# Kernel optimization log

Hardware: AMD Instinct MI355X
Metric: run time of the kernel (lower is better)

## Reference

```python
import jax, jax.numpy as jnp
import numpy as np

EMBED_DIM = 1024
HEAD_DIM = 128

def setup_inputs() -> dict:
    key = jax.random.key(0)
    ks = jax.random.split(key, 7)
    B, S = 4, 2048
    x = jax.random.normal(ks[0], (B, S, EMBED_DIM), dtype=jnp.float32)
    # Linear params: weight [embed_dim, head_dim] (applied as x @ W + b), scaled init
    scale = 1.0 / np.sqrt(EMBED_DIM)
    Wq = jax.random.normal(ks[1], (EMBED_DIM, HEAD_DIM), dtype=jnp.float32) * scale
    Wk = jax.random.normal(ks[2], (EMBED_DIM, HEAD_DIM), dtype=jnp.float32) * scale
    Wv = jax.random.normal(ks[3], (EMBED_DIM, HEAD_DIM), dtype=jnp.float32) * scale
    bq = jax.random.normal(ks[4], (HEAD_DIM,), dtype=jnp.float32) * 0.01
    bk = jax.random.normal(ks[5], (HEAD_DIM,), dtype=jnp.float32) * 0.01
    bv = jax.random.normal(ks[6], (HEAD_DIM,), dtype=jnp.float32) * 0.01
    return {"x": x, "Wq": Wq, "bq": bq, "Wk": Wk, "bk": bk, "Wv": Wv, "bv": bv}

def reference(x, Wq, bq, Wk, bk, Wv, bv):
    # x: [B, S, E]
    S = x.shape[1]
    norm = jnp.asarray(HEAD_DIM ** 0.5, x.dtype)
    q = x @ Wq + bq  # [B, S, D]
    k = x @ Wk + bk
    v = x @ Wv + bv
    scores = jnp.einsum('bsd,btd->bst', q, k) / norm  # [B, S, S]
    causal = jnp.tril(jnp.ones((S, S), dtype=bool))
    scores = jnp.where(causal, scores, -jnp.inf)
    att = jax.nn.softmax(scores, axis=-1)
    return jnp.einsum('bst,btd->bsd', att, v)  # [B, S, D]
```

## Files before the change

### kernel.cpp

```cpp
#include <hip/hip_runtime.h>
#include <hip/hip_bf16.h>

typedef __attribute__((ext_vector_type(8))) short short8;
typedef __attribute__((ext_vector_type(4))) float f32x4;

static __device__ __forceinline__ unsigned short f2bf(float f){
  union { float f; unsigned int u; } v; v.f = f;
  unsigned int r = v.u + 0x7fffu + ((v.u >> 16) & 1u);
  return (unsigned short)(r >> 16);
}

static __device__ __forceinline__ void load_lds16(const unsigned short* g, unsigned short* l){
  __builtin_amdgcn_global_load_lds(
      (const __attribute__((address_space(1))) unsigned int*)(g),
      (__attribute__((address_space(3))) unsigned int*)(l), 16, 0, 0);
}

__global__ void k_prep(const float* __restrict__ x, unsigned short* __restrict__ xb,
                       const float* __restrict__ Wq, const float* __restrict__ Wk,
                       const float* __restrict__ Wv,
                       const float* __restrict__ bq, const float* __restrict__ bk,
                       const float* __restrict__ bv,
                       unsigned short* __restrict__ Wt, float* __restrict__ bias){
  int bx = blockIdx.x;
  int tid = threadIdx.x;
  if (bx < 4096){
    int i = (bx * 256 + tid) * 8;
    float4 a = *(const float4*)(x + i);
    float4 b = *(const float4*)(x + i + 4);
    unsigned short h[8];
    h[0]=f2bf(a.x); h[1]=f2bf(a.y); h[2]=f2bf(a.z); h[3]=f2bf(a.w);
    h[4]=f2bf(b.x); h[5]=f2bf(b.y); h[6]=f2bf(b.z); h[7]=f2bf(b.w);
    *(uint4*)(xb + i) = *(uint4*)h;
  } else {
    int gid = (bx - 4096) * 256 + tid;
    int p = gid >> 17;
    int rem = gid & 131071;
    int d = rem >> 10, e = rem & 1023;
    const float* W = (p==0) ? Wq : ((p==1) ? Wk : Wv);
    Wt[gid] = f2bf(W[e*128 + d]);
    if (gid < 384){
      int pp = gid >> 7, dd = gid & 127;
      bias[gid] = (pp==0) ? bq[dd] : ((pp==1) ? bk[dd] : bv[dd]);
    }
  }
}

__global__ __launch_bounds__(256) void k_gemm_qkv(
    const unsigned short* __restrict__ Xb, const unsigned short* __restrict__ Wt,
    const float* __restrict__ bias,
    unsigned short* __restrict__ Qsw, unsigned short* __restrict__ Ksw,
    unsigned short* __restrict__ Vsw){
  __shared__ __align__(16) char smem[49152];
  float* Lf = (float*)smem;
  int tid = threadIdx.x;
  int mt = blockIdx.x;
  int p  = blockIdx.y;
  int m0 = mt * 64;
  int w = tid >> 6, lane = tid & 63, quad = lane >> 4, l16 = lane & 15;
  int wm = (w >> 1) * 32, wn = (w & 1) * 64;
  f32x4 acc[2][4];
  #pragma unroll
  for (int i=0;i<2;i++)
    #pragma unroll
    for (int j=0;j<4;j++) acc[i][j] = (f32x4){0.f,0.f,0.f,0.f};

  const unsigned short* Wp = Wt + p * (128*1024);
  const unsigned short* Ag = Xb + (m0 + w*16 + (lane>>3))*1024 + (lane&7)*8;
  const unsigned short* Bg = Wp + (w*32 + (lane>>3))*1024 + (lane&7)*8;
  int aoff = (w*16)*64;
  int boff = (w*32)*64;

  auto stage = [&](int sel, int k0){
    unsigned short* Al = (unsigned short*)(smem + sel*24576) + aoff;
    unsigned short* Bl = (unsigned short*)(smem + sel*24576 + 8192) + boff;
    load_lds16(Ag + k0, Al);
    load_lds16(Ag + k0 + 8192, Al + 512);
    #pragma unroll
    for (int s8=0; s8<4; s8++) load_lds16(Bg + k0 + s8*8192, Bl + s8*512);
  };

  stage(0, 0);
  __syncthreads();
  int cur = 0;
  for (int t=0; t<16; t++){
    if (t < 15) stage(cur^1, (t+1)*64);
    const unsigned short* Ac = (const unsigned short*)(smem + cur*24576);
    const unsigned short* Bc = Ac + 4096;
    #pragma unroll
    for (int kk=0; kk<64; kk+=32){
      short8 af[2], bf[4];
      #pragma unroll
      for (int i=0;i<2;i++) af[i] = *(const short8*)(Ac + (wm + i*16 + l16)*64 + kk + quad*8);
      #pragma unroll
      for (int j=0;j<4;j++) bf[j] = *(const short8*)(Bc + (wn + j*16 + l16)*64 + kk + quad*8);
      #pragma unroll
      for (int i=0;i<2;i++)
        #pragma unroll
        for (int j=0;j<4;j++)
          acc[i][j] = __builtin_amdgcn_mfma_f32_16x16x32_bf16(af[i], bf[j], acc[i][j], 0,0,0);
    }
    __syncthreads();
    cur ^= 1;
  }

  const float qscale = 0.08838834764831845f;
  if (p == 2){
    #pragma unroll
    for (int i=0;i<2;i++)
      #pragma unroll
      for (int j=0;j<4;j++){
        int grow0 = m0 + wm + i*16 + quad*4;
        int col = wn + j*16 + l16;
        unsigned short pk[4];
        float bv_ = bias[256 + col];
        #pragma unroll
        for (int r=0;r<4;r++) pk[r] = f2bf(acc[i][j][r] + bv_);
        int bb2 = grow0 >> 11, s = grow0 & 2047;
        int t64 = s >> 6, srem = s & 63;
        int kc2 = srem >> 5, q2 = (srem >> 3) & 3, jj = srem & 7;
        int nt = col >> 4, l2 = col & 15;
        *(uint2*)(Vsw + (bb2*32+t64)*8192 + nt*1024 + kc2*512 + q2*128 + l2*8 + jj) = *(uint2*)pk;
      }
  } else {
    #pragma unroll
    for (int i=0;i<2;i++)
      #pragma unroll
      for (int j=0;j<4;j++)
        #pragma unroll
        for (int r=0;r<4;r++)
          Lf[(wm + i*16 + quad*4 + r)*128 + wn + j*16 + l16] = acc[i][j][r];
    __syncthreads();
    unsigned short* dst = (p==0)? Qsw : Ksw;
    float scale = (p==0)? qscale : 1.0f;
    #pragma unroll
    for (int it=0; it<8; it++){
      int g = it*256 + tid;
      int row = g >> 5, cs = (g & 31)*4;
      f32x4 a = *(const f32x4*)(Lf + row*128 + cs);
      int grow = m0 + row;
      int rt = grow >> 4, m = grow & 15;
      int kc = cs >> 5, q2 = (cs >> 3) & 3, jj = cs & 7;
      unsigned short pk[4];
      #pragma unroll
      for (int k=0;k<4;k++) pk[k] = f2bf((a[k] + bias[p*128+cs+k])*scale);
      *(uint2*)(dst + rt*2048 + kc*512 + q2*128 + m*8 + jj) = *(uint2*)pk;
    }
  }
}

__global__ __launch_bounds__(64) void k_attn(
    const unsigned short* __restrict__ Qsw, const unsigned short* __restrict__ Ksw,
    const unsigned short* __restrict__ Vsw, float* __restrict__ Apart){
  __shared__ __align__(16) unsigned short Pw[16*80];
  int x = blockIdx.x;
  int b = x & 3;
  int t = x >> 2;
  int c = t & 15;
  int qb = 127 - (t >> 4);
  int T64 = (qb >> 2) + 1;
  int nch = (T64 + 1) >> 1;
  if (c >= nch) return;
  int lane = threadIdx.x;
  int quad = lane >> 4, l16 = lane & 15;
  int qs = qb * 16;

  short8 aq[4];
  #pragma unroll
  for (int kc=0;kc<4;kc++)
    aq[kc] = *(const short8*)(Qsw + (b*128 + qb)*2048 + kc*512 + lane*8);

  f32x4 o[8];
  #pragma unroll
  for (int i=0;i<8;i++) o[i] = (f32x4){0.f,0.f,0.f,0.f};
  float mcol = -1e30f;
  float lcol = 0.f;
  short8 ap[2];

  const unsigned short* Kb = Ksw + b*128*2048;
  const unsigned short* Vb = Vsw + b*32*8192;

  int tEnd = (T64 < c*2+2) ? T64 : (c*2+2);
  for (int tt = c*2; tt < tEnd; tt++){
    int t0 = tt * 64;
    f32x4 sc[4];
    #pragma unroll
    for (int nt=0;nt<4;nt++) sc[nt] = (f32x4){0.f,0.f,0.f,0.f};
    __builtin_amdgcn_s_setprio(1);
    #pragma unroll
    for (int nt=0;nt<4;nt++){
      const unsigned short* Kt = Kb + ((t0>>4)+nt)*2048 + lane*8;
      #pragma unroll
      for (int kc=0;kc<4;kc++){
        short8 kf = *(const short8*)(Kt + kc*512);
        sc[nt] = __builtin_amdgcn_mfma_f32_16x16x32_bf16(kf, aq[kc], sc[nt], 0,0,0);
      }
    }
    __builtin_amdgcn_s_setprio(0);
    if (t0 + 63 > qs){
      #pragma unroll
      for (int nt=0;nt<4;nt++){
        int kb_ = t0 + nt*16 + quad*4;
        #pragma unroll
        for (int r=0;r<4;r++)
          if (kb_ + r > qs + l16) sc[nt][r] = -1e30f;
      }
    }
    float mt_ = -1e30f;
    #pragma unroll
    for (int nt=0;nt<4;nt++)
      #pragma unroll
      for (int r=0;r<4;r++) mt_ = fmaxf(mt_, sc[nt][r]);
    mt_ = fmaxf(mt_, __shfl_xor(mt_, 16));
    mt_ = fmaxf(mt_, __shfl_xor(mt_, 32));
    float mn = fmaxf(mcol, mt_);
    float al = __expf(mcol - mn);
    mcol = mn;
    float ls = 0.f;
    #pragma unroll
    for (int nt=0;nt<4;nt++)
      #pragma unroll
      for (int r=0;r<4;r++){
        float pv = __expf(sc[nt][r] - mn);
        sc[nt][r] = pv;
        ls += pv;
      }
    ls += __shfl_xor(ls, 16);
    ls += __shfl_xor(ls, 32);
    lcol = lcol*al + ls;
    #pragma unroll
    for (int r=0;r<4;r++){
      float ar = __shfl(al, quad*4 + r);
      #pragma unroll
      for (int nt=0;nt<8;nt++) o[nt][r] *= ar;
    }
    #pragma unroll
    for (int nt=0;nt<4;nt++){
      unsigned short pk[4];
      #pragma unroll
      for (int r=0;r<4;r++) pk[r] = f2bf(sc[nt][r]);
      *(uint2*)(Pw + l16*80 + nt*16 + quad*4) = *(uint2*)pk;
    }
    ap[0] = *(const short8*)(Pw + l16*80 + quad*8);
    ap[1] = *(const short8*)(Pw + l16*80 + 32 + quad*8);
    const unsigned short* Vt0 = Vb + (t0>>6)*8192 + lane*8;
    __builtin_amdgcn_s_setprio(1);
    #pragma unroll
    for (int nt=0; nt<8; nt++)
      #pragma unroll
      for (int kc2=0;kc2<2;kc2++){
        short8 vf = *(const short8*)(Vt0 + nt*1024 + kc2*512);
        o[nt] = __builtin_amdgcn_mfma_f32_16x16x32_bf16(ap[kc2], vf, o[nt], 0,0,0);
      }
    __builtin_amdgcn_s_setprio(0);
  }

  float* slot = Apart + (size_t)((b*128 + qb)*16 + c) * 2080;
  #pragma unroll
  for (int nt=0;nt<8;nt++)
    #pragma unroll
    for (int r=0;r<4;r++)
      slot[(quad*4 + r)*128 + nt*16 + l16] = o[nt][r];
  if (quad == 0){
    slot[2048 + l16] = mcol;
    slot[2064 + l16] = lcol;
  }
}

__global__ __launch_bounds__(256) void k_acomb(const float* __restrict__ Apart,
                                               float* __restrict__ out){
  int b = blockIdx.x & 3, qb = blockIdx.x >> 2;
  int T64 = (qb >> 2) + 1;
  int nch = (T64 + 1) >> 1;
  const float* base = Apart + (size_t)((b*128 + qb)*16) * 2080;
  int tid = threadIdx.x;
  int row = tid >> 4;
  int c0 = (tid & 15) * 8;
  float m = -1e30f;
  for (int c=0;c<nch;c++) m = fmaxf(m, base[c*2080 + 2048 + row]);
  f32x4 acc[2];
  #pragma unroll
  for (int g=0;g<2;g++) acc[g] = (f32x4){0.f,0.f,0.f,0.f};
  float lsum = 0.f;
  for (int c=0;c<nch;c++){
    float e = __expf(base[c*2080 + 2048 + row] - m);
    lsum += base[c*2080 + 2064 + row] * e;
    #pragma unroll
    for (int g=0;g<2;g++){
      f32x4 v = *(const f32x4*)(base + c*2080 + row*128 + c0 + g*4);
      acc[g] += v * e;
    }
  }
  float inv = 1.0f / lsum;
  float* op = out + (size_t)(b*2048 + qb*16 + row)*128 + c0;
  #pragma unroll
  for (int g=0;g<2;g++){
    f32x4 r = acc[g] * inv;
    *(f32x4*)(op + g*4) = r;
  }
}

extern "C" void kernel_launch(void* const* d_in, const int* in_sizes, int n_in,
                              void* d_out, int out_size, void* d_ws, size_t ws_size,
                              hipStream_t stream) {
  const float* x  = (const float*)d_in[0];
  const float* Wq = (const float*)d_in[1];
  const float* bq = (const float*)d_in[2];
  const float* Wk = (const float*)d_in[3];
  const float* bk = (const float*)d_in[4];
  const float* Wv = (const float*)d_in[5];
  const float* bv = (const float*)d_in[6];
  char* ws = (char*)d_ws;
  unsigned short* Xb   = (unsigned short*)(ws);
  unsigned short* Wt   = (unsigned short*)(ws + 16777216);
  float*          bias = (float*)(ws + 17563648);
  unsigned short* Qsw  = (unsigned short*)(ws + 17565184);
  unsigned short* Ksw  = (unsigned short*)(ws + 19662336);
  unsigned short* Vsw  = (unsigned short*)(ws + 21759488);
  float*          Apart= (float*)(ws + 23856640);
  float* out = (float*)d_out;

  hipLaunchKernelGGL(k_prep,    dim3(5632),    dim3(256), 0, stream,
                     x, Xb, Wq, Wk, Wv, bq, bk, bv, Wt, bias);
  hipLaunchKernelGGL(k_gemm_qkv,dim3(128,3),   dim3(256), 0, stream,
                     Xb, Wt, bias, Qsw, Ksw, Vsw);
  hipLaunchKernelGGL(k_attn,    dim3(8192),    dim3(64),  0, stream, Qsw, Ksw, Vsw, Apart);
  hipLaunchKernelGGL(k_acomb,   dim3(512),     dim3(256), 0, stream, Apart, out);
}
```

Before: 136.8 us.

## Fuse split-K combine into attention kernel via atomic last-block reduction

Removes the separate combine kernel launch. Each attention block publishes its partial result, then increments a per-query-block atomic counter. The last block to finish merges the partials and writes the output. Query blocks with only one chunk skip the scratch buffer and write normalized output directly. This saves a launch and some global traffic, but the final combine now runs on a single 64-thread wave per query block, which adds tail work to the attention kernel.

```diff
diff --git a/kernel.cpp b/kernel.cpp
--- a/kernel.cpp
+++ b/kernel.cpp
@@ -21,7 +21,8 @@
                        const float* __restrict__ Wv,
                        const float* __restrict__ bq, const float* __restrict__ bk,
                        const float* __restrict__ bv,
-                       unsigned short* __restrict__ Wt, float* __restrict__ bias){
+                       unsigned short* __restrict__ Wt, float* __restrict__ bias,
+                       int* __restrict__ cnt){
   int bx = blockIdx.x;
   int tid = threadIdx.x;
   if (bx < 4096){
@@ -43,6 +44,7 @@
       int pp = gid >> 7, dd = gid & 127;
       bias[gid] = (pp==0) ? bq[dd] : ((pp==1) ? bk[dd] : bv[dd]);
     }
+    if (gid < 512) cnt[gid] = 0;
   }
 }
 
@@ -151,7 +153,8 @@
 
 __global__ __launch_bounds__(64) void k_attn(
     const unsigned short* __restrict__ Qsw, const unsigned short* __restrict__ Ksw,
-    const unsigned short* __restrict__ Vsw, float* __restrict__ Apart){
+    const unsigned short* __restrict__ Vsw, float* __restrict__ Apart,
+    int* __restrict__ cnt, float* __restrict__ out){
   __shared__ __align__(16) unsigned short Pw[16*80];
   int x = blockIdx.x;
   int b = x & 3;
@@ -255,7 +258,21 @@
     __builtin_amdgcn_s_setprio(0);
   }
 
-  float* slot = Apart + (size_t)((b*128 + qb)*16 + c) * 2080;
+  int gidx = b*128 + qb;
+
+  if (nch == 1){
+    float linv[4];
+    #pragma unroll
+    for (int r=0;r<4;r++) linv[r] = 1.0f / __shfl(lcol, quad*4 + r);
+    #pragma unroll
+    for (int nt=0;nt<8;nt++)
+      #pragma unroll
+      for (int r=0;r<4;r++)
+        out[(size_t)(b*2048 + qs + quad*4 + r)*128 + nt*16 + l16] = o[nt][r]*linv[r];
+    return;
+  }
+
+  float* slot = Apart + (size_t)(gidx*16 + c) * 2080;
   #pragma unroll
   for (int nt=0;nt<8;nt++)
     #pragma unroll
@@ -265,38 +282,37 @@
     slot[2048 + l16] = mcol;
     slot[2064 + l16] = lcol;
   }
-}
-
-__global__ __launch_bounds__(256) void k_acomb(const float* __restrict__ Apart,
-                                               float* __restrict__ out){
-  int b = blockIdx.x & 3, qb = blockIdx.x >> 2;
-  int T64 = (qb >> 2) + 1;
-  int nch = (T64 + 1) >> 1;
-  const float* base = Apart + (size_t)((b*128 + qb)*16) * 2080;
-  int tid = threadIdx.x;
-  int row = tid >> 4;
-  int c0 = (tid & 15) * 8;
+
+  __threadfence();
+  int old = 0;
+  if (lane == 0) old = atomicAdd(cnt + gidx, 1);
+  old = __shfl(old, 0);
+  if (old != nch - 1) return;
+  __threadfence();
+  const float* base = Apart + (size_t)(gidx*16) * 2080;
+  int row = lane >> 2;
+  int c0 = (lane & 3) * 32;
   float m = -1e30f;
-  for (int c=0;c<nch;c++) m = fmaxf(m, base[c*2080 + 2048 + row]);
-  f32x4 acc[2];
-  #pragma unroll
-  for (int g=0;g<2;g++) acc[g] = (f32x4){0.f,0.f,0.f,0.f};
+  for (int cc=0; cc<nch; cc++) m = fmaxf(m, base[cc*2080 + 2048 + row]);
+  f32x4 acc2[8];
+  #pragma unroll
+  for (int g=0;g<8;g++) acc2[g] = (f32x4){0.f,0.f,0.f,0.f};
   float lsum = 0.f;
-  for (int c=0;c<nch;c++){
-    float e = __expf(base[c*2080 + 2048 + row] - m);
-    lsum += base[c*2080 + 2064 + row] * e;
-    #pragma unroll
-    for (int g=0;g<2;g++){
-      f32x4 v = *(const f32x4*)(base + c*2080 + row*128 + c0 + g*4);
-      acc[g] += v * e;
+  for (int cc=0; cc<nch; cc++){
+    float e = __expf(base[cc*2080 + 2048 + row] - m);
+    lsum += base[cc*2080 + 2064 + row] * e;
+    #pragma unroll
+    for (int g=0;g<8;g++){
+      f32x4 v = *(const f32x4*)(base + cc*2080 + row*128 + c0 + g*4);
+      acc2[g] += v * e;
     }
   }
   float inv = 1.0f / lsum;
   float* op = out + (size_t)(b*2048 + qb*16 + row)*128 + c0;
   #pragma unroll
-  for (int g=0;g<2;g++){
-    f32x4 r = acc[g] * inv;
-    *(f32x4*)(op + g*4) = r;
+  for (int g=0;g<8;g++){
+    f32x4 rr = acc2[g] * inv;
+    *(f32x4*)(op + g*4) = rr;
   }
 }
 
@@ -318,12 +334,13 @@
   unsigned short* Ksw  = (unsigned short*)(ws + 19662336);
   unsigned short* Vsw  = (unsigned short*)(ws + 21759488);
   float*          Apart= (float*)(ws + 23856640);
+  int*            cnt  = (int*)(ws + 92014080);
   float* out = (float*)d_out;
 
   hipLaunchKernelGGL(k_prep,    dim3(5632),    dim3(256), 0, stream,
-                     x, Xb, Wq, Wk, Wv, bq, bk, bv, Wt, bias);
+                     x, Xb, Wq, Wk, Wv, bq, bk, bv, Wt, bias, cnt);
   hipLaunchKernelGGL(k_gemm_qkv,dim3(128,3),   dim3(256), 0, stream,
                      Xb, Wt, bias, Qsw, Ksw, Vsw);
-  hipLaunchKernelGGL(k_attn,    dim3(8192),    dim3(64),  0, stream, Qsw, Ksw, Vsw, Apart);
-  hipLaunchKernelGGL(k_acomb,   dim3(512),     dim3(256), 0, stream, Apart, out);
-}
+  hipLaunchKernelGGL(k_attn,    dim3(8192),    dim3(64),  0, stream,
+                     Qsw, Ksw, Vsw, Apart, cnt, out);
+}
```

New measurement: 319.3 us. 133% more time.

## Drop split-KV attention and combine kernel, one workgroup per query block

Applied to the files above, without the earlier changes.

Removes the split-KV partitioning of the attention kernel, where up to 16 chunks per query block wrote partial outputs that a separate combine kernel merged. Each 64-thread workgroup now walks the full causal key range for its 16-row query block and writes normalized output directly. This drops the partial-buffer traffic and one kernel launch. In exchange it launches only 512 single-wave workgroups with very unequal loop lengths, so parallelism and load balance fall sharply.

```diff
diff --git a/kernel.cpp b/kernel.cpp
--- a/kernel.cpp
+++ b/kernel.cpp
@@ -151,16 +151,12 @@
 
 __global__ __launch_bounds__(64) void k_attn(
     const unsigned short* __restrict__ Qsw, const unsigned short* __restrict__ Ksw,
-    const unsigned short* __restrict__ Vsw, float* __restrict__ Apart){
+    const unsigned short* __restrict__ Vsw, float* __restrict__ out){
   __shared__ __align__(16) unsigned short Pw[16*80];
   int x = blockIdx.x;
   int b = x & 3;
-  int t = x >> 2;
-  int c = t & 15;
-  int qb = 127 - (t >> 4);
+  int qb = x >> 2;
   int T64 = (qb >> 2) + 1;
-  int nch = (T64 + 1) >> 1;
-  if (c >= nch) return;
   int lane = threadIdx.x;
   int quad = lane >> 4, l16 = lane & 15;
   int qs = qb * 16;
@@ -180,8 +176,7 @@
   const unsigned short* Kb = Ksw + b*128*2048;
   const unsigned short* Vb = Vsw + b*32*8192;
 
-  int tEnd = (T64 < c*2+2) ? T64 : (c*2+2);
-  for (int tt = c*2; tt < tEnd; tt++){
+  for (int tt = 0; tt < T64; tt++){
     int t0 = tt * 64;
     f32x4 sc[4];
     #pragma unroll
@@ -255,49 +250,14 @@
     __builtin_amdgcn_s_setprio(0);
   }
 
-  float* slot = Apart + (size_t)((b*128 + qb)*16 + c) * 2080;
+  float linv[4];
+  #pragma unroll
+  for (int r=0;r<4;r++) linv[r] = 1.0f / __shfl(lcol, quad*4 + r);
   #pragma unroll
   for (int nt=0;nt<8;nt++)
     #pragma unroll
     for (int r=0;r<4;r++)
-      slot[(quad*4 + r)*128 + nt*16 + l16] = o[nt][r];
-  if (quad == 0){
-    slot[2048 + l16] = mcol;
-    slot[2064 + l16] = lcol;
-  }
-}
-
-__global__ __launch_bounds__(256) void k_acomb(const float* __restrict__ Apart,
-                                               float* __restrict__ out){
-  int b = blockIdx.x & 3, qb = blockIdx.x >> 2;
-  int T64 = (qb >> 2) + 1;
-  int nch = (T64 + 1) >> 1;
-  const float* base = Apart + (size_t)((b*128 + qb)*16) * 2080;
-  int tid = threadIdx.x;
-  int row = tid >> 4;
-  int c0 = (tid & 15) * 8;
-  float m = -1e30f;
-  for (int c=0;c<nch;c++) m = fmaxf(m, base[c*2080 + 2048 + row]);
-  f32x4 acc[2];
-  #pragma unroll
-  for (int g=0;g<2;g++) acc[g] = (f32x4){0.f,0.f,0.f,0.f};
-  float lsum = 0.f;
-  for (int c=0;c<nch;c++){
-    float e = __expf(base[c*2080 + 2048 + row] - m);
-    lsum += base[c*2080 + 2064 + row] * e;
-    #pragma unroll
-    for (int g=0;g<2;g++){
-      f32x4 v = *(const f32x4*)(base + c*2080 + row*128 + c0 + g*4);
-      acc[g] += v * e;
-    }
-  }
-  float inv = 1.0f / lsum;
-  float* op = out + (size_t)(b*2048 + qb*16 + row)*128 + c0;
-  #pragma unroll
-  for (int g=0;g<2;g++){
-    f32x4 r = acc[g] * inv;
-    *(f32x4*)(op + g*4) = r;
-  }
+      out[(size_t)(b*2048 + qs + quad*4 + r)*128 + nt*16 + l16] = o[nt][r]*linv[r];
 }
 
 extern "C" void kernel_launch(void* const* d_in, const int* in_sizes, int n_in,
@@ -317,13 +277,12 @@
   unsigned short* Qsw  = (unsigned short*)(ws + 17565184);
   unsigned short* Ksw  = (unsigned short*)(ws + 19662336);
   unsigned short* Vsw  = (unsigned short*)(ws + 21759488);
-  float*          Apart= (float*)(ws + 23856640);
   float* out = (float*)d_out;
 
   hipLaunchKernelGGL(k_prep,    dim3(5632),    dim3(256), 0, stream,
                      x, Xb, Wq, Wk, Wv, bq, bk, bv, Wt, bias);
   hipLaunchKernelGGL(k_gemm_qkv,dim3(128,3),   dim3(256), 0, stream,
                      Xb, Wt, bias, Qsw, Ksw, Vsw);
-  hipLaunchKernelGGL(k_attn,    dim3(8192),    dim3(64),  0, stream, Qsw, Ksw, Vsw, Apart);
-  hipLaunchKernelGGL(k_acomb,   dim3(512),     dim3(256), 0, stream, Apart, out);
-}
+  hipLaunchKernelGGL(k_attn,    dim3(512),     dim3(64),  0, stream,
+                     Qsw, Ksw, Vsw, out);
+}
```

Result: slower. 318.4 us (+132.7%).
